# Performance work log

Hardware: AMD Instinct MI355X
Metric: run time of the kernel (lower is better)

Reference implementation:

```python
import jax, jax.numpy as jnp
import numpy as np

TOP_K = 2
TEMP = 1.0

def setup_inputs() -> dict:
    key = jax.random.key(0)
    ks = jax.random.split(key, 7)
    B, T, D, E = 2, 2048, 768, 8
    F = 4 * D
    s = 0.02
    return {
        "x": jax.random.normal(ks[0], (B, T, D), dtype=jnp.float32),
        "gate_w": jax.random.normal(ks[1], (D, E), dtype=jnp.float32) * s,
        "gate_b": jnp.zeros((E,), dtype=jnp.float32),
        "w1": jax.random.normal(ks[2], (E, D, F), dtype=jnp.float32) * s,
        "b1": jnp.zeros((E, F), dtype=jnp.float32),
        "w2": jax.random.normal(ks[3], (E, F, D), dtype=jnp.float32) * s,
        "b2": jnp.zeros((E, D), dtype=jnp.float32),
    }

def reference(x, gate_w, gate_b, w1, b1, w2, b2):
    B, T, D = x.shape
    E = gate_w.shape[1]
    x_flat = x.reshape(-1, D)                       # [N, D]
    logits = x_flat @ gate_w + gate_b              # [N, E]
    gates = jax.nn.softmax(logits / TEMP, axis=-1)
    topk_gates, topk_idx = jax.lax.top_k(gates, TOP_K)   # [N, K]
    topk_gates = topk_gates / (jnp.sum(topk_gates, axis=-1, keepdims=True) + 1e-9)
    # Dense combine weights: w[n, e] = sum_k topk_gates[n, k] * (topk_idx[n, k] == e)
    combine = jnp.sum(
        topk_gates[:, :, None] * jax.nn.one_hot(topk_idx, E, dtype=x.dtype),
        axis=1,
    )                                               # [N, E]
    out = jnp.zeros_like(x_flat)
    for e in range(E):  # fixed small expert loop (structurally distinct params)
        h = jax.nn.gelu(x_flat @ w1[e] + b1[e], approximate=False)  # [N, 4D]
        y = h @ w2[e] + b2[e]                                       # [N, D]
        out = out + combine[:, e:e + 1] * y
    return out.reshape(B, T, D)
```

## Files before the change

### kernel.cpp

```cpp
#include <hip/hip_runtime.h>
#include <hip/hip_bf16.h>


#define N_TOK 4096
#define DIM   768
#define FDIM  3072
#define NEXP  8

typedef __attribute__((ext_vector_type(8))) _Float16 f16x8;
typedef __attribute__((ext_vector_type(4))) _Float16 f16x4;
typedef __attribute__((ext_vector_type(4))) float     f32x4;

__device__ __forceinline__ float gelu_exact(float v) {
    return 0.5f * v * (1.0f + erff(v * 0.7071067811865475f));
}

__device__ __forceinline__ void gload_lds16(const _Float16* g, _Float16* l) {
    __builtin_amdgcn_global_load_lds(
        (const __attribute__((address_space(1))) void*)g,
        (__attribute__((address_space(3))) void*)l,
        16, 0, 0);
}

__global__ __launch_bounds__(256) void cast_x_kernel(const float* __restrict__ x,
                                                     _Float16* __restrict__ xh) {
    int i = blockIdx.x * 256 + threadIdx.x;
    float4 v = ((const float4*)x)[i];
    f16x4 o;
    o[0] = (_Float16)v.x; o[1] = (_Float16)v.y;
    o[2] = (_Float16)v.z; o[3] = (_Float16)v.w;
    ((f16x4*)xh)[i] = o;
}

__global__ __launch_bounds__(256) void transpose_cast2_kernel(const float* __restrict__ w1,
                                                              const float* __restrict__ w2,
                                                              _Float16* __restrict__ w1t,
                                                              _Float16* __restrict__ w2t) {
    const int z     = blockIdx.y;
    const int which = z >> 3;
    const int e     = z & 7;
    const float* in; _Float16* out; int R, C, tx, ty;
    if (which == 0) { in = w1; out = w1t; R = DIM;  C = FDIM; tx = blockIdx.x % (FDIM / 64); ty = blockIdx.x / (FDIM / 64); }
    else            { in = w2; out = w2t; R = FDIM; C = DIM;  tx = blockIdx.x % (DIM  / 64); ty = blockIdx.x / (DIM  / 64); }
    const size_t eoff = (size_t)e * R * C;
    const int c0 = tx * 64;
    const int r0 = ty * 64;
    __shared__ _Float16 tile[64][66];
    const int t = threadIdx.x;
    #pragma unroll
    for (int it = 0; it < 4; it++) {
        int lin = it * 256 + t;
        int r  = lin >> 4;
        int c4 = lin & 15;
        float4 v = *(const float4*)&in[eoff + (size_t)(r0 + r) * C + c0 + c4 * 4];
        tile[r][c4 * 4 + 0] = (_Float16)v.x;
        tile[r][c4 * 4 + 1] = (_Float16)v.y;
        tile[r][c4 * 4 + 2] = (_Float16)v.z;
        tile[r][c4 * 4 + 3] = (_Float16)v.w;
    }
    __syncthreads();
    #pragma unroll
    for (int it = 0; it < 4; it++) {
        int lin = it * 256 + t;
        int c  = lin >> 4;
        int r4 = lin & 15;
        f16x4 o;
        #pragma unroll
        for (int j = 0; j < 4; j++) o[j] = tile[r4 * 4 + j][c];
        *(f16x4*)&out[eoff + (size_t)(c0 + c) * R + r0 + r4 * 4] = o;
    }
}

__global__ __launch_bounds__(256) void gate_kernel(const float* __restrict__ x,
                                                   const float* __restrict__ gw,
                                                   const float* __restrict__ gb,
                                                   int* __restrict__ tok_list,
                                                   float* __restrict__ wt_list,
                                                   int* __restrict__ count) {
    const int gtid = blockIdx.x * 256 + threadIdx.x;
    const int n    = gtid >> 6;
    const int lane = threadIdx.x & 63;
    if (n >= N_TOK) return;
    double part[NEXP];
    #pragma unroll
    for (int e = 0; e < NEXP; e++) part[e] = 0.0;
    for (int d = lane; d < DIM; d += 64) {
        float xv = x[n * DIM + d];
        const float* g = &gw[d * NEXP];
        #pragma unroll
        for (int e = 0; e < NEXP; e++) part[e] += (double)xv * (double)g[e];
    }
    #pragma unroll
    for (int e = 0; e < NEXP; e++) {
        double v = part[e];
        #pragma unroll
        for (int off = 32; off > 0; off >>= 1) v += __shfl_xor(v, off);
        part[e] = v + (double)gb[e];
    }
    if (lane == 0) {
        double mx = part[0];
        #pragma unroll
        for (int e = 1; e < NEXP; e++) mx = fmax(mx, part[e]);
        double ex[NEXP]; double s = 0.0;
        #pragma unroll
        for (int e = 0; e < NEXP; e++) { ex[e] = exp(part[e] - mx); s += ex[e]; }
        int i0 = 0;
        #pragma unroll
        for (int e = 1; e < NEXP; e++) if (ex[e] > ex[i0]) i0 = e;
        int i1 = (i0 == 0) ? 1 : 0;
        #pragma unroll
        for (int e = 0; e < NEXP; e++) if (e != i0 && ex[e] > ex[i1]) i1 = e;
        float g0 = (float)(ex[i0] / s), g1 = (float)(ex[i1] / s);
        float dn = g0 + g1 + 1e-9f;
        float w0 = g0 / dn, w1 = g1 / dn;
        int s0 = atomicAdd(&count[i0], 1);
        tok_list[i0 * N_TOK + s0] = n;  wt_list[i0 * N_TOK + s0] = w0;
        int s1 = atomicAdd(&count[i1], 1);
        tok_list[i1 * N_TOK + s1] = n;  wt_list[i1 * N_TOK + s1] = w1;
    }
}

__global__ void scan_kernel(const int* __restrict__ count, int* __restrict__ basep) {
    if (threadIdx.x == 0) {
        int s = 0;
        for (int e = 0; e < NEXP; e++) { basep[e] = s; s += count[e]; }
    }
}

__global__ __launch_bounds__(256) void mm1_kernel(const _Float16* __restrict__ xh,
                                                  const _Float16* __restrict__ w1t,
                                                  const float* __restrict__ bias1,
                                                  const int* __restrict__ tok_list,
                                                  const int* __restrict__ count,
                                                  const int* __restrict__ basep,
                                                  _Float16* __restrict__ h) {
    const int e    = blockIdx.y;
    const int cnt  = count[e];
    const int row0 = blockIdx.z * 128;
    if (row0 >= cnt) return;
    const int col0 = blockIdx.x * 128;
    const int t    = threadIdx.x;
    const int lane = t & 63;
    const int wv   = t >> 6;
    const int wy   = wv >> 1, wx = wv & 1;
    const int m_lane = lane & 15, quad = lane >> 4;

    __shared__ __align__(16) _Float16 As[128][64];
    __shared__ __align__(16) _Float16 Bs[128][64];

    const int srow    = t >> 3;
    const int kin     = (t & 7) * 8;
    const int kin_src = ((t & 7) ^ (srow & 7)) * 8;

    const _Float16* pa[4];
    #pragma unroll
    for (int g = 0; g < 4; g++) {
        int i = row0 + g * 32 + srow; if (i > cnt - 1) i = cnt - 1;
        pa[g] = xh + (size_t)tok_list[e * N_TOK + i] * DIM + kin_src;
    }
    const _Float16* pb[4];
    #pragma unroll
    for (int g = 0; g < 4; g++)
        pb[g] = w1t + (size_t)e * FDIM * DIM + (size_t)(col0 + g * 32 + srow) * DIM + kin_src;

    f32x4 acc[4][4];
    #pragma unroll
    for (int i = 0; i < 4; i++)
        #pragma unroll
        for (int j = 0; j < 4; j++)
            acc[i][j] = (f32x4){0.f, 0.f, 0.f, 0.f};

    const int rsw = (m_lane & 7);

    for (int kk = 0; kk < DIM; kk += 64) {
        __syncthreads();
        #pragma unroll
        for (int g = 0; g < 4; g++) gload_lds16(pa[g] + kk, &As[g * 32 + srow][kin]);
        #pragma unroll
        for (int g = 0; g < 4; g++) gload_lds16(pb[g] + kk, &Bs[g * 32 + srow][kin]);
        __syncthreads();
        #pragma unroll
        for (int ks = 0; ks < 2; ks++) {
            const int rc = ((ks * 4 + quad) ^ rsw) * 8;
            f16x8 af[4], bf[4];
            #pragma unroll
            for (int i = 0; i < 4; i++)
                af[i] = *(const f16x8*)&As[wy * 64 + i * 16 + m_lane][rc];
            #pragma unroll
            for (int j = 0; j < 4; j++)
                bf[j] = *(const f16x8*)&Bs[wx * 64 + j * 16 + m_lane][rc];
            #pragma unroll
            for (int i = 0; i < 4; i++)
                #pragma unroll
                for (int j = 0; j < 4; j++)
                    acc[i][j] = __builtin_amdgcn_mfma_f32_16x16x32_f16(af[i], bf[j], acc[i][j], 0, 0, 0);
        }
    }

    const int hbase = basep[e];
    #pragma unroll
    for (int i = 0; i < 4; i++) {
        #pragma unroll
        for (int r = 0; r < 4; r++) {
            int rl = wy * 64 + i * 16 + quad * 4 + r;
            int gr = row0 + rl;
            if (gr < cnt) {
                _Float16* hrow = h + (size_t)(hbase + gr) * FDIM;
                #pragma unroll
                for (int j = 0; j < 4; j++) {
                    int c = col0 + wx * 64 + j * 16 + m_lane;
                    float v = acc[i][j][r] + bias1[e * FDIM + c];
                    hrow[c] = (_Float16)gelu_exact(v);
                }
            }
        }
    }
}

__global__ __launch_bounds__(256) void mm2_kernel(const _Float16* __restrict__ h,
                                                  const _Float16* __restrict__ w2t,
                                                  const float* __restrict__ bias2,
                                                  const int* __restrict__ tok_list,
                                                  const float* __restrict__ wt_list,
                                                  const int* __restrict__ count,
                                                  const int* __restrict__ basep,
                                                  float* __restrict__ out) {
    const int e    = blockIdx.y;
    const int cnt  = count[e];
    const int row0 = blockIdx.z * 64;
    if (row0 >= cnt) return;
    const int col0 = blockIdx.x * 128;
    const int t    = threadIdx.x;
    const int lane = t & 63;
    const int wv   = t >> 6;
    const int m_lane = lane & 15, quad = lane >> 4;

    __shared__ __align__(16) _Float16 As[64][64];
    __shared__ __align__(16) _Float16 Bs[128][64];

    const int srow    = t >> 3;
    const int kin     = (t & 7) * 8;
    const int kin_src = ((t & 7) ^ (srow & 7)) * 8;

    const int hbase = basep[e];
    const _Float16* pa[2];
    #pragma unroll
    for (int g = 0; g < 2; g++) {
        int i = row0 + g * 32 + srow; if (i > cnt - 1) i = cnt - 1;
        pa[g] = h + (size_t)(hbase + i) * FDIM + kin_src;
    }
    const _Float16* pb[4];
    #pragma unroll
    for (int g = 0; g < 4; g++)
        pb[g] = w2t + (size_t)e * DIM * FDIM + (size_t)(col0 + g * 32 + srow) * FDIM + kin_src;

    f32x4 acc[4][2];
    #pragma unroll
    for (int i = 0; i < 4; i++)
        #pragma unroll
        for (int j = 0; j < 2; j++)
            acc[i][j] = (f32x4){0.f, 0.f, 0.f, 0.f};

    const int rsw = (m_lane & 7);

    for (int kk = 0; kk < FDIM; kk += 64) {
        __syncthreads();
        #pragma unroll
        for (int g = 0; g < 2; g++) gload_lds16(pa[g] + kk, &As[g * 32 + srow][kin]);
        #pragma unroll
        for (int g = 0; g < 4; g++) gload_lds16(pb[g] + kk, &Bs[g * 32 + srow][kin]);
        __syncthreads();
        #pragma unroll
        for (int ks = 0; ks < 2; ks++) {
            const int rc = ((ks * 4 + quad) ^ rsw) * 8;
            f16x8 af[4], bf[2];
            #pragma unroll
            for (int i = 0; i < 4; i++)
                af[i] = *(const f16x8*)&As[i * 16 + m_lane][rc];
            #pragma unroll
            for (int j = 0; j < 2; j++)
                bf[j] = *(const f16x8*)&Bs[wv * 32 + j * 16 + m_lane][rc];
            #pragma unroll
            for (int i = 0; i < 4; i++)
                #pragma unroll
                for (int j = 0; j < 2; j++)
                    acc[i][j] = __builtin_amdgcn_mfma_f32_16x16x32_f16(af[i], bf[j], acc[i][j], 0, 0, 0);
        }
    }

    #pragma unroll
    for (int i = 0; i < 4; i++) {
        #pragma unroll
        for (int r = 0; r < 4; r++) {
            int rl = i * 16 + quad * 4 + r;
            int gr = row0 + rl;
            if (gr < cnt) {
                int tok   = tok_list[e * N_TOK + gr];
                float wgt = wt_list[e * N_TOK + gr];
                float* orow = out + (size_t)tok * DIM;
                #pragma unroll
                for (int j = 0; j < 2; j++) {
                    int c = col0 + wv * 32 + j * 16 + m_lane;
                    float v = acc[i][j][r] + bias2[e * DIM + c];
                    atomicAdd(&orow[c], wgt * v);
                }
            }
        }
    }
}

extern "C" void kernel_launch(void* const* d_in, const int* in_sizes, int n_in,
                              void* d_out, int out_size, void* d_ws, size_t ws_size,
                              hipStream_t stream) {
    const float* x  = (const float*)d_in[0];
    const float* gw = (const float*)d_in[1];
    const float* gb = (const float*)d_in[2];
    const float* w1 = (const float*)d_in[3];
    const float* b1 = (const float*)d_in[4];
    const float* w2 = (const float*)d_in[5];
    const float* b2 = (const float*)d_in[6];
    float* out = (float*)d_out;

    char* ws = (char*)d_ws;
    _Float16* xh   = (_Float16*)ws;
    _Float16* w1t  = xh  + (size_t)N_TOK * DIM;
    _Float16* w2t  = w1t + (size_t)NEXP * FDIM * DIM;
    _Float16* hbuf = w2t + (size_t)NEXP * DIM * FDIM;
    int*   tok_list = (int*)(hbuf + (size_t)2 * N_TOK * FDIM);
    float* wt_list  = (float*)(tok_list + NEXP * N_TOK);
    int*   count    = (int*)(wt_list + NEXP * N_TOK);
    int*   basep    = count + 8;

    hipMemsetAsync(count, 0, 64, stream);
    hipMemsetAsync(out, 0, (size_t)out_size * sizeof(float), stream);

    cast_x_kernel<<<dim3(N_TOK * DIM / 4 / 256), 256, 0, stream>>>(x, xh);
    transpose_cast2_kernel<<<dim3(576, 16), 256, 0, stream>>>(w1, w2, w1t, w2t);
    gate_kernel<<<dim3(N_TOK / 4), 256, 0, stream>>>(x, gw, gb, tok_list, wt_list, count);
    scan_kernel<<<1, 64, 0, stream>>>(count, basep);
    mm1_kernel<<<dim3(FDIM / 128, NEXP, N_TOK / 128), 256, 0, stream>>>(
        xh, w1t, b1, tok_list, count, basep, hbuf);
    mm2_kernel<<<dim3(DIM / 128, NEXP, N_TOK / 64), 256, 0, stream>>>(
        hbuf, w2t, b2, tok_list, wt_list, count, basep, out);
}
```

Before: 486.6 us.

## Fuse preprocessing kernels into one launch, drop scan, vectorize mm1 epilogue

Folds the x cast, the weight transpose-cast and the gating/top-k routing into a single block-partitioned pre_kernel, and removes the scan kernel by having each GEMM block compute its expert offset from the counts. It cuts the number of launches and lets the independent preprocessing stages run concurrently. The mm1 MFMA operands are swapped so each lane holds four consecutive columns, which allows float4 bias loads and 8-byte f16x4 stores of h instead of scalar ones. The per-block prefix sum adds a little redundant work, and a single large grid may schedule less evenly.

```diff
diff --git a/kernel.cpp b/kernel.cpp
--- a/kernel.cpp
+++ b/kernel.cpp
@@ -6,6 +6,11 @@
 #define DIM   768
 #define FDIM  3072
 #define NEXP  8
+
+#define TRANS_BLOCKS 9216
+#define GATE_BLOCKS  1024
+#define CAST_BLOCKS  3072
+#define PRE_BLOCKS   (TRANS_BLOCKS + GATE_BLOCKS + CAST_BLOCKS)
 
 typedef __attribute__((ext_vector_type(8))) _Float16 f16x8;
 typedef __attribute__((ext_vector_type(4))) _Float16 f16x4;
@@ -22,108 +27,103 @@
         16, 0, 0);
 }
 
-__global__ __launch_bounds__(256) void cast_x_kernel(const float* __restrict__ x,
-                                                     _Float16* __restrict__ xh) {
-    int i = blockIdx.x * 256 + threadIdx.x;
-    float4 v = ((const float4*)x)[i];
-    f16x4 o;
-    o[0] = (_Float16)v.x; o[1] = (_Float16)v.y;
-    o[2] = (_Float16)v.z; o[3] = (_Float16)v.w;
-    ((f16x4*)xh)[i] = o;
-}
-
-__global__ __launch_bounds__(256) void transpose_cast2_kernel(const float* __restrict__ w1,
-                                                              const float* __restrict__ w2,
-                                                              _Float16* __restrict__ w1t,
-                                                              _Float16* __restrict__ w2t) {
-    const int z     = blockIdx.y;
-    const int which = z >> 3;
-    const int e     = z & 7;
-    const float* in; _Float16* out; int R, C, tx, ty;
-    if (which == 0) { in = w1; out = w1t; R = DIM;  C = FDIM; tx = blockIdx.x % (FDIM / 64); ty = blockIdx.x / (FDIM / 64); }
-    else            { in = w2; out = w2t; R = FDIM; C = DIM;  tx = blockIdx.x % (DIM  / 64); ty = blockIdx.x / (DIM  / 64); }
-    const size_t eoff = (size_t)e * R * C;
-    const int c0 = tx * 64;
-    const int r0 = ty * 64;
-    __shared__ _Float16 tile[64][66];
-    const int t = threadIdx.x;
-    #pragma unroll
-    for (int it = 0; it < 4; it++) {
-        int lin = it * 256 + t;
-        int r  = lin >> 4;
-        int c4 = lin & 15;
-        float4 v = *(const float4*)&in[eoff + (size_t)(r0 + r) * C + c0 + c4 * 4];
-        tile[r][c4 * 4 + 0] = (_Float16)v.x;
-        tile[r][c4 * 4 + 1] = (_Float16)v.y;
-        tile[r][c4 * 4 + 2] = (_Float16)v.z;
-        tile[r][c4 * 4 + 3] = (_Float16)v.w;
-    }
-    __syncthreads();
-    #pragma unroll
-    for (int it = 0; it < 4; it++) {
-        int lin = it * 256 + t;
-        int c  = lin >> 4;
-        int r4 = lin & 15;
+__global__ __launch_bounds__(256) void pre_kernel(const float* __restrict__ x,
+                                                  const float* __restrict__ gw,
+                                                  const float* __restrict__ gb,
+                                                  const float* __restrict__ w1,
+                                                  const float* __restrict__ w2,
+                                                  _Float16* __restrict__ xh,
+                                                  _Float16* __restrict__ w1t,
+                                                  _Float16* __restrict__ w2t,
+                                                  int* __restrict__ tok_list,
+                                                  float* __restrict__ wt_list,
+                                                  int* __restrict__ count) {
+    const int bid = blockIdx.x;
+    const int t   = threadIdx.x;
+
+    if (bid < TRANS_BLOCKS) {
+        const int z     = bid & 15;
+        const int xx    = bid >> 4;
+        const int which = z >> 3;
+        const int e     = z & 7;
+        const float* in; _Float16* out; int R, C, tx, ty;
+        if (which == 0) { in = w1; out = w1t; R = DIM;  C = FDIM; tx = xx % (FDIM / 64); ty = xx / (FDIM / 64); }
+        else            { in = w2; out = w2t; R = FDIM; C = DIM;  tx = xx % (DIM  / 64); ty = xx / (DIM  / 64); }
+        const size_t eoff = (size_t)e * R * C;
+        const int c0 = tx * 64;
+        const int r0 = ty * 64;
+        __shared__ _Float16 tile[64][66];
+        #pragma unroll
+        for (int it = 0; it < 4; it++) {
+            int lin = it * 256 + t;
+            int r  = lin >> 4;
+            int c4 = lin & 15;
+            float4 v = *(const float4*)&in[eoff + (size_t)(r0 + r) * C + c0 + c4 * 4];
+            tile[r][c4 * 4 + 0] = (_Float16)v.x;
+            tile[r][c4 * 4 + 1] = (_Float16)v.y;
+            tile[r][c4 * 4 + 2] = (_Float16)v.z;
+            tile[r][c4 * 4 + 3] = (_Float16)v.w;
+        }
+        __syncthreads();
+        #pragma unroll
+        for (int it = 0; it < 4; it++) {
+            int lin = it * 256 + t;
+            int c  = lin >> 4;
+            int r4 = lin & 15;
+            f16x4 o;
+            #pragma unroll
+            for (int j = 0; j < 4; j++) o[j] = tile[r4 * 4 + j][c];
+            *(f16x4*)&out[eoff + (size_t)(c0 + c) * R + r0 + r4 * 4] = o;
+        }
+    } else if (bid < TRANS_BLOCKS + GATE_BLOCKS) {
+        const int gtid = (bid - TRANS_BLOCKS) * 256 + t;
+        const int n    = gtid >> 6;
+        const int lane = t & 63;
+        if (n >= N_TOK) return;
+        double part[NEXP];
+        #pragma unroll
+        for (int e = 0; e < NEXP; e++) part[e] = 0.0;
+        for (int d = lane; d < DIM; d += 64) {
+            float xv = x[n * DIM + d];
+            const float* g = &gw[d * NEXP];
+            #pragma unroll
+            for (int e = 0; e < NEXP; e++) part[e] += (double)xv * (double)g[e];
+        }
+        #pragma unroll
+        for (int e = 0; e < NEXP; e++) {
+            double v = part[e];
+            #pragma unroll
+            for (int off = 32; off > 0; off >>= 1) v += __shfl_xor(v, off);
+            part[e] = v + (double)gb[e];
+        }
+        if (lane == 0) {
+            double mx = part[0];
+            #pragma unroll
+            for (int e = 1; e < NEXP; e++) mx = fmax(mx, part[e]);
+            double ex[NEXP]; double s = 0.0;
+            #pragma unroll
+            for (int e = 0; e < NEXP; e++) { ex[e] = exp(part[e] - mx); s += ex[e]; }
+            int i0 = 0;
+            #pragma unroll
+            for (int e = 1; e < NEXP; e++) if (ex[e] > ex[i0]) i0 = e;
+            int i1 = (i0 == 0) ? 1 : 0;
+            #pragma unroll
+            for (int e = 0; e < NEXP; e++) if (e != i0 && ex[e] > ex[i1]) i1 = e;
+            float g0 = (float)(ex[i0] / s), g1 = (float)(ex[i1] / s);
+            float dn = g0 + g1 + 1e-9f;
+            float w0 = g0 / dn, w1v = g1 / dn;
+            int s0 = atomicAdd(&count[i0], 1);
+            tok_list[i0 * N_TOK + s0] = n;  wt_list[i0 * N_TOK + s0] = w0;
+            int s1 = atomicAdd(&count[i1], 1);
+            tok_list[i1 * N_TOK + s1] = n;  wt_list[i1 * N_TOK + s1] = w1v;
+        }
+    } else {
+        const int i = (bid - TRANS_BLOCKS - GATE_BLOCKS) * 256 + t;
+        float4 v = ((const float4*)x)[i];
         f16x4 o;
-        #pragma unroll
-        for (int j = 0; j < 4; j++) o[j] = tile[r4 * 4 + j][c];
-        *(f16x4*)&out[eoff + (size_t)(c0 + c) * R + r0 + r4 * 4] = o;
-    }
-}
-
-__global__ __launch_bounds__(256) void gate_kernel(const float* __restrict__ x,
-                                                   const float* __restrict__ gw,
-                                                   const float* __restrict__ gb,
-                                                   int* __restrict__ tok_list,
-                                                   float* __restrict__ wt_list,
-                                                   int* __restrict__ count) {
-    const int gtid = blockIdx.x * 256 + threadIdx.x;
-    const int n    = gtid >> 6;
-    const int lane = threadIdx.x & 63;
-    if (n >= N_TOK) return;
-    double part[NEXP];
-    #pragma unroll
-    for (int e = 0; e < NEXP; e++) part[e] = 0.0;
-    for (int d = lane; d < DIM; d += 64) {
-        float xv = x[n * DIM + d];
-        const float* g = &gw[d * NEXP];
-        #pragma unroll
-        for (int e = 0; e < NEXP; e++) part[e] += (double)xv * (double)g[e];
-    }
-    #pragma unroll
-    for (int e = 0; e < NEXP; e++) {
-        double v = part[e];
-        #pragma unroll
-        for (int off = 32; off > 0; off >>= 1) v += __shfl_xor(v, off);
-        part[e] = v + (double)gb[e];
-    }
-    if (lane == 0) {
-        double mx = part[0];
-        #pragma unroll
-        for (int e = 1; e < NEXP; e++) mx = fmax(mx, part[e]);
-        double ex[NEXP]; double s = 0.0;
-        #pragma unroll
-        for (int e = 0; e < NEXP; e++) { ex[e] = exp(part[e] - mx); s += ex[e]; }
-        int i0 = 0;
-        #pragma unroll
-        for (int e = 1; e < NEXP; e++) if (ex[e] > ex[i0]) i0 = e;
-        int i1 = (i0 == 0) ? 1 : 0;
-        #pragma unroll
-        for (int e = 0; e < NEXP; e++) if (e != i0 && ex[e] > ex[i1]) i1 = e;
-        float g0 = (float)(ex[i0] / s), g1 = (float)(ex[i1] / s);
-        float dn = g0 + g1 + 1e-9f;
-        float w0 = g0 / dn, w1 = g1 / dn;
-        int s0 = atomicAdd(&count[i0], 1);
-        tok_list[i0 * N_TOK + s0] = n;  wt_list[i0 * N_TOK + s0] = w0;
-        int s1 = atomicAdd(&count[i1], 1);
-        tok_list[i1 * N_TOK + s1] = n;  wt_list[i1 * N_TOK + s1] = w1;
-    }
-}
-
-__global__ void scan_kernel(const int* __restrict__ count, int* __restrict__ basep) {
-    if (threadIdx.x == 0) {
-        int s = 0;
-        for (int e = 0; e < NEXP; e++) { basep[e] = s; s += count[e]; }
+        o[0] = (_Float16)v.x; o[1] = (_Float16)v.y;
+        o[2] = (_Float16)v.z; o[3] = (_Float16)v.w;
+        ((f16x4*)xh)[i] = o;
     }
 }
 
@@ -132,7 +132,6 @@
                                                   const float* __restrict__ bias1,
                                                   const int* __restrict__ tok_list,
                                                   const int* __restrict__ count,
-                                                  const int* __restrict__ basep,
                                                   _Float16* __restrict__ h) {
     const int e    = blockIdx.y;
     const int cnt  = count[e];
@@ -193,25 +192,28 @@
             for (int i = 0; i < 4; i++)
                 #pragma unroll
                 for (int j = 0; j < 4; j++)
-                    acc[i][j] = __builtin_amdgcn_mfma_f32_16x16x32_f16(af[i], bf[j], acc[i][j], 0, 0, 0);
-        }
-    }
-
-    const int hbase = basep[e];
+                    acc[i][j] = __builtin_amdgcn_mfma_f32_16x16x32_f16(bf[j], af[i], acc[i][j], 0, 0, 0);
+        }
+    }
+
+    int hbase = 0;
+    for (int q = 0; q < NEXP; q++) if (q < e) hbase += count[q];
+
     #pragma unroll
     for (int i = 0; i < 4; i++) {
-        #pragma unroll
-        for (int r = 0; r < 4; r++) {
-            int rl = wy * 64 + i * 16 + quad * 4 + r;
-            int gr = row0 + rl;
-            if (gr < cnt) {
-                _Float16* hrow = h + (size_t)(hbase + gr) * FDIM;
-                #pragma unroll
-                for (int j = 0; j < 4; j++) {
-                    int c = col0 + wx * 64 + j * 16 + m_lane;
-                    float v = acc[i][j][r] + bias1[e * FDIM + c];
-                    hrow[c] = (_Float16)gelu_exact(v);
-                }
+        int gr = row0 + wy * 64 + i * 16 + m_lane;
+        if (gr < cnt) {
+            _Float16* hrow = h + (size_t)(hbase + gr) * FDIM;
+            #pragma unroll
+            for (int j = 0; j < 4; j++) {
+                int c = col0 + wx * 64 + j * 16 + quad * 4;
+                float4 b4 = *(const float4*)&bias1[e * FDIM + c];
+                f16x4 o;
+                o[0] = (_Float16)gelu_exact(acc[i][j][0] + b4.x);
+                o[1] = (_Float16)gelu_exact(acc[i][j][1] + b4.y);
+                o[2] = (_Float16)gelu_exact(acc[i][j][2] + b4.z);
+                o[3] = (_Float16)gelu_exact(acc[i][j][3] + b4.w);
+                *(f16x4*)&hrow[c] = o;
             }
         }
     }
@@ -223,7 +225,6 @@
                                                   const int* __restrict__ tok_list,
                                                   const float* __restrict__ wt_list,
                                                   const int* __restrict__ count,
-                                                  const int* __restrict__ basep,
                                                   float* __restrict__ out) {
     const int e    = blockIdx.y;
     const int cnt  = count[e];
@@ -242,7 +243,9 @@
     const int kin     = (t & 7) * 8;
     const int kin_src = ((t & 7) ^ (srow & 7)) * 8;
 
-    const int hbase = basep[e];
+    int hbase = 0;
+    for (int q = 0; q < NEXP; q++) if (q < e) hbase += count[q];
+
     const _Float16* pa[2];
     #pragma unroll
     for (int g = 0; g < 2; g++) {
@@ -329,17 +332,15 @@
     int*   tok_list = (int*)(hbuf + (size_t)2 * N_TOK * FDIM);
     float* wt_list  = (float*)(tok_list + NEXP * N_TOK);
     int*   count    = (int*)(wt_list + NEXP * N_TOK);
-    int*   basep    = count + 8;
 
     hipMemsetAsync(count, 0, 64, stream);
     hipMemsetAsync(out, 0, (size_t)out_size * sizeof(float), stream);
 
-    cast_x_kernel<<<dim3(N_TOK * DIM / 4 / 256), 256, 0, stream>>>(x, xh);
-    transpose_cast2_kernel<<<dim3(576, 16), 256, 0, stream>>>(w1, w2, w1t, w2t);
-    gate_kernel<<<dim3(N_TOK / 4), 256, 0, stream>>>(x, gw, gb, tok_list, wt_list, count);
-    scan_kernel<<<1, 64, 0, stream>>>(count, basep);
+    pre_kernel<<<dim3(PRE_BLOCKS), 256, 0, stream>>>(
+        x, gw, gb, w1, w2, xh, w1t, w2t, tok_list, wt_list, count);
+
     mm1_kernel<<<dim3(FDIM / 128, NEXP, N_TOK / 128), 256, 0, stream>>>(
-        xh, w1t, b1, tok_list, count, basep, hbuf);
+        xh, w1t, b1, tok_list, count, hbuf);
     mm2_kernel<<<dim3(DIM / 128, NEXP, N_TOK / 64), 256, 0, stream>>>(
-        hbuf, w2t, b2, tok_list, wt_list, count, basep, out);
-}
+        hbuf, w2t, b2, tok_list, wt_list, count, out);
+}
```

Measured after the change: 456.7 us. 6.1% less time.
